# Kernel optimization log

Hardware: AMD Instinct MI355X
Metric: run time of the kernel (lower is better)

## Reference

```python
import jax, jax.numpy as jnp
import numpy as np

EPS = 1e-6
TTT_BASE_LR = 1.0
NUM_HEADS = 16


def _ln_fused_l2_bwd(x, l2_target, gamma, beta, eps=EPS):
    # Gradient of ||LN(x)*gamma+beta - target||^2/2 wrt x (fused LN + L2 bwd).
    mu = x.mean(axis=-1, keepdims=True)
    var = ((x - mu) ** 2).mean(axis=-1, keepdims=True)
    std = jnp.sqrt(var + eps)
    x_hat = (x - mu) / std
    grad_x_hat = (gamma * x_hat + beta - l2_target) * gamma
    z = (grad_x_hat
         - grad_x_hat.mean(axis=-1, keepdims=True)
         - x_hat * (grad_x_hat * x_hat).mean(axis=-1, keepdims=True)) / std
    return z


def _ln_fwd(x, gamma, beta, eps=EPS):
    mu = x.mean(axis=-1, keepdims=True)
    var = ((x - mu) ** 2).mean(axis=-1, keepdims=True)
    x_hat = (x - mu) / jnp.sqrt(var + eps)
    return gamma * x_hat + beta


def setup_inputs() -> dict:
    key = jax.random.key(0)
    ks = jax.random.split(key, 6)
    B, L, C, H = 2, 2048, 1024, NUM_HEADS
    D = C // H
    return {
        "hidden_states": jax.random.normal(ks[0], (B, L, C), jnp.float32),
        "Wq": jax.random.normal(ks[1], (C, C), jnp.float32) * 0.02,
        "Wk": jax.random.normal(ks[2], (C, C), jnp.float32) * 0.02,
        "Wv": jax.random.normal(ks[3], (C, C), jnp.float32) * 0.02,
        "W1": jax.random.normal(ks[4], (H, D, D), jnp.float32) * 0.02,
        "b1": jnp.zeros((H, 1, D), jnp.float32),
        "ttt_norm_weight": jnp.ones((H, D), jnp.float32),
        "ttt_norm_bias": jnp.zeros((H, D), jnp.float32),
        "lr_weight": jax.random.normal(ks[5], (H, C, 1), jnp.float32) * 0.02,
        "lr_bias": jnp.zeros((H, 1), jnp.float32),
    }


def reference(hidden_states, Wq, Wk, Wv, W1, b1,
              ttt_norm_weight, ttt_norm_bias, lr_weight, lr_bias):
    B, L, C = hidden_states.shape
    H = NUM_HEADS
    D = C // H

    def proj(W):  # nn.Linear(no bias): x @ W^T, then split heads -> [B,H,L,D]
        return (hidden_states @ W.T).reshape(B, L, H, D).transpose(0, 2, 1, 3)

    XQ, XK, XV = proj(Wq), proj(Wk), proj(Wv)

    # adaptive per-token learning rate eta: [B,H,L,1]
    ttt_lr = jnp.einsum("blc,hci->bhli", hidden_states, lr_weight)
    ttt_lr = jax.nn.sigmoid(ttt_lr + lr_bias.reshape(1, H, 1, 1))
    eta = TTT_BASE_LR * ttt_lr / D

    # inner-loop forward with initial fast weights W1,b1
    Z1 = jnp.einsum("bhld,hdf->bhlf", XK, W1) + b1[None]  # [B,H,L,D]
    recon_target = XV - XK

    gamma = ttt_norm_weight.reshape(1, H, 1, D)
    beta = ttt_norm_bias.reshape(1, H, 1, D)
    grad_l_wrt_Z1 = _ln_fused_l2_bwd(Z1, recon_target, gamma, beta)

    # dual form update (batch-parallel, no state carry)
    eg = eta * grad_l_wrt_Z1                               # [B,H,L,D]
    Attn1 = jnp.einsum("bhld,bhmd->bhlm", XQ, XK)          # [B,H,L,L]
    b1_bar = b1[None] - eg.sum(axis=2, keepdims=True)      # [B,H,1,D]
    Z1_bar = (jnp.einsum("bhld,hdf->bhlf", XQ, W1)
              - jnp.einsum("bhlm,bhmd->bhld", Attn1, eg)
              + b1_bar)

    Z1_normalized = _ln_fwd(Z1_bar, gamma, beta)
    return XQ + Z1_normalized  # [B,H,L,D]
```

## Files before the change

kernel.cpp:

```cpp
#include <hip/hip_runtime.h>
#include <math.h>

#define B_ 2
#define L_ 2048
#define C_ 1024
#define H_ 16
#define D_ 64
#define BH_ (B_*H_)
#define M_ (B_*L_)
#define N_ (3*C_)
#define K_ C_
#define EPS_ 1e-6f
#define NCHUNK_ 16
#define LDT_ 136
#define WTS_ 72

typedef unsigned short ushort_t;
typedef short short8 __attribute__((ext_vector_type(8)));
typedef float f32x4 __attribute__((ext_vector_type(4)));
typedef unsigned short ushort4_t __attribute__((ext_vector_type(4)));

__device__ __forceinline__ ushort_t f2bf(float f) {
    union { float f; unsigned u; } v; v.f = f;
    unsigned r = v.u + 0x7FFFu + ((v.u >> 16) & 1u);
    return (ushort_t)(r >> 16);
}
__device__ __forceinline__ float bf2f(ushort_t h) {
    union { unsigned u; float f; } v; v.u = ((unsigned)h) << 16;
    return v.f;
}

__device__ __forceinline__ void gload16(const void* g, void* l) {
    __builtin_amdgcn_global_load_lds(
        (const __attribute__((address_space(1))) void*)g,
        (__attribute__((address_space(3))) void*)l, 16, 0, 0);
}

__global__ __launch_bounds__(256) void cast_eta(
    const float* __restrict__ hs, const float* __restrict__ Wq,
    const float* __restrict__ Wk, const float* __restrict__ Wv,
    const float* __restrict__ W1, const float* __restrict__ lrw,
    const float* __restrict__ lrb, ushort_t* __restrict__ hsB,
    ushort_t* __restrict__ Wcat, float* __restrict__ eta,
    ushort_t* __restrict__ W1tg, float* __restrict__ W1tf) {
    __shared__ float pA[16][257], pB[16][257];
    const int bid = blockIdx.x, t = threadIdx.x;
    if (bid < 2048) {
        const int iA = bid * 2, iB = iA + 1;
        const float* rA = hs + (size_t)iA * C_;
        const float* rB = hs + (size_t)iB * C_;
        f32x4 a = *(const f32x4*)(rA + t * 4);
        f32x4 b = *(const f32x4*)(rB + t * 4);
        ushort4_t oa, ob;
        oa.x = f2bf(a.x); oa.y = f2bf(a.y); oa.z = f2bf(a.z); oa.w = f2bf(a.w);
        ob.x = f2bf(b.x); ob.y = f2bf(b.y); ob.z = f2bf(b.z); ob.w = f2bf(b.w);
        *(ushort4_t*)(hsB + (size_t)iA * C_ + t * 4) = oa;
        *(ushort4_t*)(hsB + (size_t)iB * C_ + t * 4) = ob;
        #pragma unroll
        for (int h = 0; h < 16; ++h) {
            f32x4 w = *(const f32x4*)(lrw + (size_t)h * C_ + t * 4);
            pA[h][t] = a.x * w.x + a.y * w.y + a.z * w.z + a.w * w.w;
            pB[h][t] = b.x * w.x + b.y * w.y + b.z * w.z + b.w * w.w;
        }
        __syncthreads();
        const int h = t >> 4, seg = t & 15;
        float sA = 0.f, sB = 0.f;
        #pragma unroll
        for (int j = 0; j < 16; ++j) {
            sA += pA[h][seg * 16 + j];
            sB += pB[h][seg * 16 + j];
        }
        #pragma unroll
        for (int m = 1; m < 16; m <<= 1) {
            sA += __shfl_xor(sA, m, 64);
            sB += __shfl_xor(sB, m, 64);
        }
        if (seg == 0) {
            float bb = lrb[h];
            int bA = iA >> 11, lA = iA & (L_ - 1);
            int bB = iB >> 11, lB = iB & (L_ - 1);
            eta[((size_t)(bA * H_ + h)) * L_ + lA] =
                (1.f / (1.f + expf(-(sA + bb)))) * (1.0f / 64.0f);
            eta[((size_t)(bB * H_ + h)) * L_ + lB] =
                (1.f / (1.f + expf(-(sB + bb)))) * (1.0f / 64.0f);
        }
    } else if (bid < 2816) {
        const int wb = bid - 2048;
        #pragma unroll
        for (int ii = 0; ii < 4; ++ii) {
            int cid = wb * 1024 + ii * 256 + t;
            int m = cid >> 18, r = cid & ((1 << 18) - 1);
            f32x4 v;
            if (m == 0)      v = *(const f32x4*)(Wq + (size_t)r * 4);
            else if (m == 1) v = *(const f32x4*)(Wk + (size_t)r * 4);
            else {
                f32x4 vv = *(const f32x4*)(Wv + (size_t)r * 4);
                f32x4 vk = *(const f32x4*)(Wk + (size_t)r * 4);
                v.x = vv.x - vk.x; v.y = vv.y - vk.y;
                v.z = vv.z - vk.z; v.w = vv.w - vk.w;
            }
            ushort4_t o;
            o.x = f2bf(v.x); o.y = f2bf(v.y); o.z = f2bf(v.z); o.w = f2bf(v.w);
            *(ushort4_t*)(Wcat + (size_t)m * (C_ * C_) + (size_t)r * 4) = o;
        }
    } else {
        const int h = bid - 2816;
        __shared__ float Wl[64 * 65];
        #pragma unroll
        for (int p = 0; p < 4; ++p) {
            int i4 = p * 256 + t;
            int e = i4 >> 4, f0 = (i4 & 15) * 4;
            f32x4 v = *(const f32x4*)(W1 + (size_t)h * 4096 + e * 64 + f0);
            Wl[(f0 + 0) * 65 + e] = v.x;
            Wl[(f0 + 1) * 65 + e] = v.y;
            Wl[(f0 + 2) * 65 + e] = v.z;
            Wl[(f0 + 3) * 65 + e] = v.w;
        }
        __syncthreads();
        #pragma unroll
        for (int p = 0; p < 16; ++p) {
            int flat = p * 256 + t;
            float v = Wl[(flat >> 6) * 65 + (flat & 63)];
            W1tf[(size_t)h * 4096 + flat] = v;
            W1tg[(size_t)h * 4096 + flat] = f2bf(v);
        }
    }
}

__global__ __launch_bounds__(256) void gemm_qkv(
    const ushort_t* __restrict__ A, const ushort_t* __restrict__ Bc,
    ushort_t* __restrict__ XQ, ushort_t* __restrict__ XK,
    ushort_t* __restrict__ XT) {
    __shared__ __align__(16) ushort_t Al[128 * 32];
    __shared__ __align__(16) ushort_t Bl[128 * 32];
    const int bm = blockIdx.x, bn = blockIdx.y;
    const int t = threadIdx.x, w = t >> 6, lane = t & 63;
    const int wr = w >> 1, wc = w & 1;
    const int la15 = lane & 15, la4 = lane >> 4;
    f32x4 acc[4][4];
    #pragma unroll
    for (int a = 0; a < 4; a++)
        #pragma unroll
        for (int b = 0; b < 4; b++)
            #pragma unroll
            for (int j = 0; j < 4; j++) acc[a][b][j] = 0.f;

    const int ci0 = w * 64 + lane;
    const int xread = (la15 >> 1) & 3;
    const int uslot = la4 ^ xread;

    for (int kt = 0; kt < K_ / 32; ++kt) {
        __syncthreads();
        #pragma unroll
        for (int q = 0; q < 2; ++q) {
            int ci = q * 256 + ci0;
            int r = ci >> 2, kc = ci & 3;
            int kcp = kc ^ ((r >> 1) & 3);
            gload16(A + (size_t)(bm * 128 + r) * K_ + kt * 32 + kcp * 8,
                    &Al[q * 2048 + w * 512]);
            gload16(Bc + (size_t)(bn * 128 + r) * K_ + kt * 32 + kcp * 8,
                    &Bl[q * 2048 + w * 512]);
        }
        __syncthreads();
        short8 af[4], bfv[4];
        #pragma unroll
        for (int mf = 0; mf < 4; ++mf)
            af[mf] = *(const short8*)&Al[(wr * 64 + mf * 16 + la15) * 32 + uslot * 8];
        #pragma unroll
        for (int nf = 0; nf < 4; ++nf)
            bfv[nf] = *(const short8*)&Bl[(wc * 64 + nf * 16 + la15) * 32 + uslot * 8];
        #pragma unroll
        for (int mf = 0; mf < 4; ++mf)
            #pragma unroll
            for (int nf = 0; nf < 4; ++nf)
                acc[mf][nf] = __builtin_amdgcn_mfma_f32_16x16x32_bf16(
                    af[mf], bfv[nf], acc[mf][nf], 0, 0, 0);
    }

    const int jbase = bn * 128;
    const int mtx = jbase >> 10;
    ushort_t* dst = (mtx == 0) ? XQ : (mtx == 1 ? XK : XT);
    #pragma unroll
    for (int mf = 0; mf < 4; ++mf)
        #pragma unroll
        for (int nf = 0; nf < 4; ++nf)
            #pragma unroll
            for (int rg = 0; rg < 4; ++rg) {
                int i = bm * 128 + wr * 64 + mf * 16 + (la4 << 2) + rg;
                int j = (jbase & 1023) + wc * 64 + nf * 16 + la15;
                int b = i >> 11, l = i & (L_ - 1);
                int h = j >> 6, d = j & 63;
                dst[((size_t)(b * H_ + h) * L_ + l) * D_ + d] = f2bf(acc[mf][nf][rg]);
            }
}

__global__ __launch_bounds__(512) void k2_grad2(
    const ushort_t* __restrict__ XK, const ushort_t* __restrict__ XT,
    const ushort_t* __restrict__ W1tg, const float* __restrict__ b1,
    const float* __restrict__ tw, const float* __restrict__ tb,
    const float* __restrict__ eta, float* __restrict__ GpT,
    float* __restrict__ bsump) {
    __shared__ __align__(16) ushort_t xkt[64 * LDT_];
    __shared__ __align__(16) ushort_t egl[64 * LDT_];
    __shared__ float b1s[64], gs[64], bes[64];
    __shared__ float sred[8][64];
    const int bh = blockIdx.y, lt = blockIdx.x;
    const int h = bh & (H_ - 1);
    const int t = threadIdx.x, w = t >> 6, lane = t & 63;
    const int la15 = lane & 15, la4 = lane >> 4;
    if (t < 64) { b1s[t] = b1[h * 64 + t]; gs[t] = tw[h * 64 + t]; bes[t] = tb[h * 64 + t]; }
    __syncthreads();

    const ushort_t* xk = XK + (size_t)bh * L_ * D_;
    const ushort_t* xt = XT + (size_t)bh * L_ * D_;
    const ushort_t* w1g = W1tg + (size_t)h * 4096;
    const int l0 = lt * 128 + w * 16;
    const int llw = w * 16;

    f32x4 acc[4];
    #pragma unroll
    for (int nf = 0; nf < 4; nf++) {
        float bv = b1s[nf * 16 + la15];
        #pragma unroll
        for (int j = 0; j < 4; j++) acc[nf][j] = bv;
    }
    #pragma unroll
    for (int ks = 0; ks < 2; ++ks) {
        short8 af, bfv[4];
        const int d0 = ks * 32 + la4 * 8;
        af = *(const short8*)&xk[(size_t)(l0 + la15) * D_ + d0];
        {
            const int ll = llw + la15;
            #pragma unroll
            for (int jj = 0; jj < 8; jj++)
                xkt[(d0 + jj) * LDT_ + ll] = (ushort_t)af[jj];
        }
        #pragma unroll
        for (int nf = 0; nf < 4; nf++)
            bfv[nf] = *(const short8*)&w1g[(nf * 16 + la15) * 64 + d0];
        #pragma unroll
        for (int nf = 0; nf < 4; nf++)
            acc[nf] = __builtin_amdgcn_mfma_f32_16x16x32_bf16(
                af, bfv[nf], acc[nf], 0, 0, 0);
    }

    const float* etap = eta + (size_t)bh * L_;
    float accbs[4] = {0.f, 0.f, 0.f, 0.f};
    #pragma unroll
    for (int rg = 0; rg < 4; ++rg) {
        int lrow = l0 + (la4 << 2) + rg;
        int llr  = llw + (la4 << 2) + rg;
        float x[4], xh[4], gh[4];
        #pragma unroll
        for (int nf = 0; nf < 4; nf++) x[nf] = acc[nf][rg];
        float s = x[0] + x[1] + x[2] + x[3];
        float q = x[0]*x[0] + x[1]*x[1] + x[2]*x[2] + x[3]*x[3];
        s += __shfl_xor(s, 1, 64); q += __shfl_xor(q, 1, 64);
        s += __shfl_xor(s, 2, 64); q += __shfl_xor(q, 2, 64);
        s += __shfl_xor(s, 4, 64); q += __shfl_xor(q, 4, 64);
        s += __shfl_xor(s, 8, 64); q += __shfl_xor(q, 8, 64);
        float mu = s * (1.f / 64.f);
        float var = q * (1.f / 64.f) - mu * mu;
        float inv = 1.f / sqrtf(var + EPS_);
        float s1 = 0.f, s2 = 0.f;
        #pragma unroll
        for (int nf = 0; nf < 4; nf++) {
            int d = nf * 16 + la15;
            xh[nf] = (x[nf] - mu) * inv;
            float tgt = bf2f(xt[(size_t)lrow * D_ + d]);
            float g = gs[d];
            gh[nf] = (g * xh[nf] + bes[d] - tgt) * g;
            s1 += gh[nf]; s2 += gh[nf] * xh[nf];
        }
        s1 += __shfl_xor(s1, 1, 64); s2 += __shfl_xor(s2, 1, 64);
        s1 += __shfl_xor(s1, 2, 64); s2 += __shfl_xor(s2, 2, 64);
        s1 += __shfl_xor(s1, 4, 64); s2 += __shfl_xor(s2, 4, 64);
        s1 += __shfl_xor(s1, 8, 64); s2 += __shfl_xor(s2, 8, 64);
        float m1 = s1 * (1.f / 64.f), m2 = s2 * (1.f / 64.f);
        float el = etap[lrow];
        #pragma unroll
        for (int nf = 0; nf < 4; nf++) {
            int d = nf * 16 + la15;
            float egv = el * ((gh[nf] - m1 - xh[nf] * m2) * inv);
            accbs[nf] += egv;
            egl[d * LDT_ + llr] = f2bf(egv);
        }
    }
    #pragma unroll
    for (int nf = 0; nf < 4; nf++) {
        accbs[nf] += __shfl_xor(accbs[nf], 16, 64);
        accbs[nf] += __shfl_xor(accbs[nf], 32, 64);
    }
    if (lane < 16)
        #pragma unroll
        for (int nf = 0; nf < 4; nf++) sred[w][nf * 16 + lane] = accbs[nf];
    __syncthreads();

    if (w < 4) {
        f32x4 aG[4];
        #pragma unroll
        for (int nf = 0; nf < 4; nf++)
            #pragma unroll
            for (int j = 0; j < 4; j++) aG[nf][j] = 0.f;
        #pragma unroll
        for (int ks = 0; ks < 4; ++ks) {
            const int ko = ks * 32 + la4 * 8;
            short8 ae = *(const short8*)&egl[(w * 16 + la15) * LDT_ + ko];
            #pragma unroll
            for (int nf = 0; nf < 4; nf++) {
                short8 be = *(const short8*)&xkt[(nf * 16 + la15) * LDT_ + ko];
                aG[nf] = __builtin_amdgcn_mfma_f32_16x16x32_bf16(ae, be, aG[nf], 0, 0, 0);
            }
        }
        float* gp = GpT + (size_t)(bh * NCHUNK_ + lt) * 4096;
        #pragma unroll
        for (int nf = 0; nf < 4; nf++)
            #pragma unroll
            for (int rg = 0; rg < 4; rg++) {
                int f = w * 16 + (la4 << 2) + rg;
                int e = nf * 16 + la15;
                gp[f * 64 + e] = aG[nf][rg];
            }
    }
    if (t < 64) {
        float s = 0.f;
        #pragma unroll
        for (int ww = 0; ww < 8; ww++) s += sred[ww][t];
        bsump[(bh * NCHUNK_ + lt) * 64 + t] = s;
    }
}

__global__ __launch_bounds__(256) void k2b_reduce(
    const float* __restrict__ GpT, const float* __restrict__ bsump,
    float* __restrict__ G, float* __restrict__ bsum) {
    const int seg = blockIdx.x, bh = blockIdx.y;
    const int t = threadIdx.x;
    #pragma unroll 2
    for (int ii = 0; ii < 2; ++ii) {
        int i = seg * 512 + ii * 256 + t;
        float s = 0.f;
        #pragma unroll
        for (int c = 0; c < NCHUNK_; c++)
            s += GpT[(size_t)(bh * NCHUNK_ + c) * 4096 + i];
        G[(size_t)bh * 4096 + i] = s;
    }
    if (seg == 0 && t < 64) {
        float s = 0.f;
        #pragma unroll
        for (int c = 0; c < NCHUNK_; c++)
            s += bsump[(bh * NCHUNK_ + c) * 64 + t];
        bsum[bh * 64 + t] = s;
    }
}

__global__ __launch_bounds__(512) void k3_out(
    const ushort_t* __restrict__ XQ, const float* __restrict__ W1tf,
    const float* __restrict__ G, const float* __restrict__ b1,
    const float* __restrict__ bsum, const float* __restrict__ tw,
    const float* __restrict__ tb, float* __restrict__ out) {
    __shared__ __align__(16) ushort_t Wt[64 * WTS_];
    __shared__ float b1s[64], gs[64], bes[64];
    const int bh = blockIdx.y, lt = blockIdx.x;
    const int h = bh & (H_ - 1);
    const int t = threadIdx.x, w = t >> 6, lane = t & 63;
    const int la15 = lane & 15, la4 = lane >> 4;
    for (int p = t; p < 4096; p += 512) {
        float s = W1tf[(size_t)h * 4096 + p] - G[(size_t)bh * 4096 + p];
        Wt[(p >> 6) * WTS_ + (p & 63)] = f2bf(s);
    }
    if (t < 64) {
        b1s[t] = b1[h * 64 + t] - bsum[bh * 64 + t];
        gs[t] = tw[h * 64 + t]; bes[t] = tb[h * 64 + t];
    }
    __syncthreads();

    const ushort_t* xq = XQ + (size_t)bh * L_ * D_;
    const int l0 = lt * 128 + w * 16;
    f32x4 acc[4];
    #pragma unroll
    for (int nf = 0; nf < 4; nf++) {
        float bv = b1s[nf * 16 + la15];
        #pragma unroll
        for (int j = 0; j < 4; j++) acc[nf][j] = bv;
    }
    #pragma unroll
    for (int ks = 0; ks < 2; ++ks) {
        short8 af, bfv[4];
        const int d0 = ks * 32 + la4 * 8;
        af = *(const short8*)&xq[(size_t)(l0 + la15) * D_ + d0];
        #pragma unroll
        for (int nf = 0; nf < 4; nf++)
            bfv[nf] = *(const short8*)&Wt[(nf * 16 + la15) * WTS_ + d0];
        #pragma unroll
        for (int nf = 0; nf < 4; nf++)
            acc[nf] = __builtin_amdgcn_mfma_f32_16x16x32_bf16(
                af, bfv[nf], acc[nf], 0, 0, 0);
    }

    float* outp = out + (size_t)bh * L_ * D_;
    #pragma unroll
    for (int rg = 0; rg < 4; ++rg) {
        int lrow = l0 + (la4 << 2) + rg;
        float x[4];
        #pragma unroll
        for (int nf = 0; nf < 4; nf++) x[nf] = acc[nf][rg];
        float s = x[0] + x[1] + x[2] + x[3];
        float q = x[0]*x[0] + x[1]*x[1] + x[2]*x[2] + x[3]*x[3];
        s += __shfl_xor(s, 1, 64); q += __shfl_xor(q, 1, 64);
        s += __shfl_xor(s, 2, 64); q += __shfl_xor(q, 2, 64);
        s += __shfl_xor(s, 4, 64); q += __shfl_xor(q, 4, 64);
        s += __shfl_xor(s, 8, 64); q += __shfl_xor(q, 8, 64);
        float mu = s * (1.f / 64.f);
        float var = q * (1.f / 64.f) - mu * mu;
        float inv = 1.f / sqrtf(var + EPS_);
        #pragma unroll
        for (int nf = 0; nf < 4; nf++) {
            int d = nf * 16 + la15;
            float xh = (x[nf] - mu) * inv;
            float o = gs[d] * xh + bes[d];
            float qv = bf2f(xq[(size_t)lrow * D_ + d]);
            outp[(size_t)lrow * D_ + d] = qv + o;
        }
    }
}

extern "C" void kernel_launch(void* const* d_in, const int* in_sizes, int n_in,
                              void* d_out, int out_size, void* d_ws, size_t ws_size,
                              hipStream_t stream) {
    const float* hs  = (const float*)d_in[0];
    const float* Wq  = (const float*)d_in[1];
    const float* Wk  = (const float*)d_in[2];
    const float* Wv  = (const float*)d_in[3];
    const float* W1  = (const float*)d_in[4];
    const float* b1  = (const float*)d_in[5];
    const float* tw  = (const float*)d_in[6];
    const float* tb  = (const float*)d_in[7];
    const float* lrw = (const float*)d_in[8];
    const float* lrb = (const float*)d_in[9];
    float* out = (float*)d_out;

    char* ws = (char*)d_ws;
    size_t off = 0;
    ushort_t* hsB  = (ushort_t*)(ws + off); off += (size_t)M_ * K_ * 2;
    ushort_t* Wcat = (ushort_t*)(ws + off); off += (size_t)N_ * K_ * 2;
    ushort_t* XQ   = (ushort_t*)(ws + off); off += (size_t)M_ * C_ * 2;
    ushort_t* XK   = (ushort_t*)(ws + off); off += (size_t)M_ * C_ * 2;
    ushort_t* XT   = (ushort_t*)(ws + off); off += (size_t)M_ * C_ * 2;
    float*    eta  = (float*)(ws + off);    off += (size_t)BH_ * L_ * 4;
    ushort_t* W1tg = (ushort_t*)(ws + off); off += (size_t)H_ * D_ * D_ * 2;
    float*    W1tf = (float*)(ws + off);    off += (size_t)H_ * D_ * D_ * 4;
    float*    G    = (float*)(ws + off);    off += (size_t)BH_ * D_ * D_ * 4;
    float*    bsum = (float*)(ws + off);    off += (size_t)BH_ * D_ * 4;
    float*    GpT   = (float*)hsB;
    float*    bsump = (float*)Wcat;

    cast_eta<<<2048 + 768 + 16, 256, 0, stream>>>(hs, Wq, Wk, Wv, W1, lrw, lrb,
                                                  hsB, Wcat, eta, W1tg, W1tf);
    gemm_qkv<<<dim3(M_ / 128, N_ / 128), 256, 0, stream>>>(hsB, Wcat, XQ, XK, XT);
    k2_grad2<<<dim3(L_ / 128, BH_), 512, 0, stream>>>(XK, XT, W1tg, b1, tw, tb, eta, GpT, bsump);
    k2b_reduce<<<dim3(8, BH_), 256, 0, stream>>>(GpT, bsump, G, bsum);
    k3_out<<<dim3(L_ / 128, BH_), 512, 0, stream>>>(XQ, W1tf, G, b1, bsum, tw, tb, out);
}
```

Before: 74.84 us.

## Fold learning-rate projection into QKV GEMM as an extra output tile column

Drops the per-row learning-rate dot product and LDS reduction from the cast kernel. Instead lr_weight is appended to the bf16 weight matrix as 16 extra rows, padded into a 25th column tile of the QKV GEMM, whose epilogue applies the sigmoid and writes eta. This makes the cast kernel a plain streaming conversion, at the cost of one extra GEMM tile column that mostly computes padding. eta now comes from bf16 inputs, so it loses some precision.

```diff
diff --git a/kernel.cpp b/kernel.cpp
--- a/kernel.cpp
+++ b/kernel.cpp
@@ -9,6 +9,7 @@
 #define BH_ (B_*H_)
 #define M_ (B_*L_)
 #define N_ (3*C_)
+#define NW_ 3200
 #define K_ C_
 #define EPS_ 1e-6f
 #define NCHUNK_ 16
@@ -36,55 +37,24 @@
         (__attribute__((address_space(3))) void*)l, 16, 0, 0);
 }
 
-__global__ __launch_bounds__(256) void cast_eta(
+__global__ __launch_bounds__(256) void cast_w(
     const float* __restrict__ hs, const float* __restrict__ Wq,
     const float* __restrict__ Wk, const float* __restrict__ Wv,
     const float* __restrict__ W1, const float* __restrict__ lrw,
-    const float* __restrict__ lrb, ushort_t* __restrict__ hsB,
-    ushort_t* __restrict__ Wcat, float* __restrict__ eta,
+    ushort_t* __restrict__ hsB, ushort_t* __restrict__ Wcat,
     ushort_t* __restrict__ W1tg, float* __restrict__ W1tf) {
-    __shared__ float pA[16][257], pB[16][257];
     const int bid = blockIdx.x, t = threadIdx.x;
     if (bid < 2048) {
-        const int iA = bid * 2, iB = iA + 1;
-        const float* rA = hs + (size_t)iA * C_;
-        const float* rB = hs + (size_t)iB * C_;
-        f32x4 a = *(const f32x4*)(rA + t * 4);
-        f32x4 b = *(const f32x4*)(rB + t * 4);
-        ushort4_t oa, ob;
-        oa.x = f2bf(a.x); oa.y = f2bf(a.y); oa.z = f2bf(a.z); oa.w = f2bf(a.w);
-        ob.x = f2bf(b.x); ob.y = f2bf(b.y); ob.z = f2bf(b.z); ob.w = f2bf(b.w);
-        *(ushort4_t*)(hsB + (size_t)iA * C_ + t * 4) = oa;
-        *(ushort4_t*)(hsB + (size_t)iB * C_ + t * 4) = ob;
-        #pragma unroll
-        for (int h = 0; h < 16; ++h) {
-            f32x4 w = *(const f32x4*)(lrw + (size_t)h * C_ + t * 4);
-            pA[h][t] = a.x * w.x + a.y * w.y + a.z * w.z + a.w * w.w;
-            pB[h][t] = b.x * w.x + b.y * w.y + b.z * w.z + b.w * w.w;
-        }
-        __syncthreads();
-        const int h = t >> 4, seg = t & 15;
-        float sA = 0.f, sB = 0.f;
-        #pragma unroll
-        for (int j = 0; j < 16; ++j) {
-            sA += pA[h][seg * 16 + j];
-            sB += pB[h][seg * 16 + j];
-        }
-        #pragma unroll
-        for (int m = 1; m < 16; m <<= 1) {
-            sA += __shfl_xor(sA, m, 64);
-            sB += __shfl_xor(sB, m, 64);
-        }
-        if (seg == 0) {
-            float bb = lrb[h];
-            int bA = iA >> 11, lA = iA & (L_ - 1);
-            int bB = iB >> 11, lB = iB & (L_ - 1);
-            eta[((size_t)(bA * H_ + h)) * L_ + lA] =
-                (1.f / (1.f + expf(-(sA + bb)))) * (1.0f / 64.0f);
-            eta[((size_t)(bB * H_ + h)) * L_ + lB] =
-                (1.f / (1.f + expf(-(sB + bb)))) * (1.0f / 64.0f);
-        }
-    } else if (bid < 2816) {
+        const int iA = bid * 2;
+        #pragma unroll
+        for (int rr = 0; rr < 2; ++rr) {
+            const float* r = hs + (size_t)(iA + rr) * C_;
+            f32x4 a = *(const f32x4*)(r + t * 4);
+            ushort4_t o;
+            o.x = f2bf(a.x); o.y = f2bf(a.y); o.z = f2bf(a.z); o.w = f2bf(a.w);
+            *(ushort4_t*)(hsB + (size_t)(iA + rr) * C_ + t * 4) = o;
+        }
+    } else if (bid < 2820) {
         const int wb = bid - 2048;
         #pragma unroll
         for (int ii = 0; ii < 4; ++ii) {
@@ -93,18 +63,20 @@
             f32x4 v;
             if (m == 0)      v = *(const f32x4*)(Wq + (size_t)r * 4);
             else if (m == 1) v = *(const f32x4*)(Wk + (size_t)r * 4);
-            else {
+            else if (m == 2) {
                 f32x4 vv = *(const f32x4*)(Wv + (size_t)r * 4);
                 f32x4 vk = *(const f32x4*)(Wk + (size_t)r * 4);
                 v.x = vv.x - vk.x; v.y = vv.y - vk.y;
                 v.z = vv.z - vk.z; v.w = vv.w - vk.w;
+            } else {
+                v = *(const f32x4*)(lrw + (size_t)r * 4);
             }
             ushort4_t o;
             o.x = f2bf(v.x); o.y = f2bf(v.y); o.z = f2bf(v.z); o.w = f2bf(v.w);
             *(ushort4_t*)(Wcat + (size_t)m * (C_ * C_) + (size_t)r * 4) = o;
         }
     } else {
-        const int h = bid - 2816;
+        const int h = bid - 2820;
         __shared__ float Wl[64 * 65];
         #pragma unroll
         for (int p = 0; p < 4; ++p) {
@@ -130,7 +102,8 @@
 __global__ __launch_bounds__(256) void gemm_qkv(
     const ushort_t* __restrict__ A, const ushort_t* __restrict__ Bc,
     ushort_t* __restrict__ XQ, ushort_t* __restrict__ XK,
-    ushort_t* __restrict__ XT) {
+    ushort_t* __restrict__ XT, const float* __restrict__ lrb,
+    float* __restrict__ eta) {
     __shared__ __align__(16) ushort_t Al[128 * 32];
     __shared__ __align__(16) ushort_t Bl[128 * 32];
     const int bm = blockIdx.x, bn = blockIdx.y;
@@ -175,6 +148,23 @@
             for (int nf = 0; nf < 4; ++nf)
                 acc[mf][nf] = __builtin_amdgcn_mfma_f32_16x16x32_bf16(
                     af[mf], bfv[nf], acc[mf][nf], 0, 0, 0);
+    }
+
+    if (bn == 24) {
+        if (wc == 0) {
+            const float bb = lrb[la15];
+            #pragma unroll
+            for (int mf = 0; mf < 4; ++mf)
+                #pragma unroll
+                for (int rg = 0; rg < 4; ++rg) {
+                    int i = bm * 128 + wr * 64 + mf * 16 + la4 * 4 + rg;
+                    int b = i >> 11, l = i & (L_ - 1);
+                    float x = acc[mf][0][rg] + bb;
+                    eta[((size_t)(b * H_ + la15)) * L_ + l] =
+                        (1.f / (1.f + expf(-x))) * (1.0f / 64.0f);
+                }
+        }
+        return;
     }
 
     const int jbase = bn * 128;
@@ -442,7 +432,7 @@
     char* ws = (char*)d_ws;
     size_t off = 0;
     ushort_t* hsB  = (ushort_t*)(ws + off); off += (size_t)M_ * K_ * 2;
-    ushort_t* Wcat = (ushort_t*)(ws + off); off += (size_t)N_ * K_ * 2;
+    ushort_t* Wcat = (ushort_t*)(ws + off); off += (size_t)NW_ * K_ * 2;
     ushort_t* XQ   = (ushort_t*)(ws + off); off += (size_t)M_ * C_ * 2;
     ushort_t* XK   = (ushort_t*)(ws + off); off += (size_t)M_ * C_ * 2;
     ushort_t* XT   = (ushort_t*)(ws + off); off += (size_t)M_ * C_ * 2;
@@ -454,9 +444,9 @@
     float*    GpT   = (float*)hsB;
     float*    bsump = (float*)Wcat;
 
-    cast_eta<<<2048 + 768 + 16, 256, 0, stream>>>(hs, Wq, Wk, Wv, W1, lrw, lrb,
-                                                  hsB, Wcat, eta, W1tg, W1tf);
-    gemm_qkv<<<dim3(M_ / 128, N_ / 128), 256, 0, stream>>>(hsB, Wcat, XQ, XK, XT);
+    cast_w<<<2048 + 772 + 16, 256, 0, stream>>>(hs, Wq, Wk, Wv, W1, lrw,
+                                                hsB, Wcat, W1tg, W1tf);
+    gemm_qkv<<<dim3(M_ / 128, 25), 256, 0, stream>>>(hsB, Wcat, XQ, XK, XT, lrb, eta);
     k2_grad2<<<dim3(L_ / 128, BH_), 512, 0, stream>>>(XK, XT, W1tg, b1, tw, tb, eta, GpT, bsump);
     k2b_reduce<<<dim3(8, BH_), 256, 0, stream>>>(GpT, bsump, G, bsum);
     k3_out<<<dim3(L_ / 128, BH_), 512, 0, stream>>>(XQ, W1tf, G, b1, bsum, tw, tb, out);
```

Result: slower. 83.20 us (+11.2%).
